# Kernel tuning notes

Hardware: AMD Instinct MI355X
Metric: run time of the kernel (lower is better)

## Reference

```python
import jax, jax.numpy as jnp
import numpy as np


def setup_inputs() -> dict:
    key = jax.random.key(0)
    ks = jax.random.split(key, 10)
    B, S, I, H, O, L = 64, 512, 256, 1024, 256, 3
    sI = 1.0 / np.sqrt(I)
    sH = 1.0 / np.sqrt(H)
    return {
        "x": jax.random.normal(ks[0], (B, S, I), jnp.float32),
        "h0": jax.random.normal(ks[1], (B, L, H), jnp.float32) * 0.1,
        "Wx0": jax.random.normal(ks[2], (I, 3 * H), jnp.float32) * sI,
        "Wh0": jax.random.normal(ks[3], (H, 3 * H), jnp.float32) * sH,
        "bh0": jax.random.normal(ks[4], (3 * H,), jnp.float32) * sH,
        "Wx": jax.random.normal(ks[5], (L - 1, H, 3 * H), jnp.float32) * sH,
        "Wh": jax.random.normal(ks[6], (L - 1, H, 3 * H), jnp.float32) * sH,
        "bh": jax.random.normal(ks[7], (L - 1, 3 * H), jnp.float32) * sH,
        "Wy": jax.random.normal(ks[8], (H, O), jnp.float32) * sH,
        "by": jax.random.normal(ks[9], (O,), jnp.float32) * sH,
    }


def _gru_forward(x, h0, Wx0, Wh0, bh0, Wx, Wh, bh, Wy, by):
    B, S, I = x.shape
    L = h0.shape[1]
    H = Wh0.shape[0]
    # per-layer params; gate order in the fused 3H dim: [z, r, g]
    params = [(Wx0, Wh0, bh0)] + [(Wx[l], Wh[l], bh[l]) for l in range(L - 1)]

    def step(states, x_t):
        states = list(states)
        cur = x_t  # (B, in_dim of layer)
        for l in range(L):
            Wx_l, Wh_l, b_l = params[l]
            h_prev = states[l]  # (B, H)
            gx = cur @ Wx_l  # (B, 3H), no bias (w_x* has bias=False)
            xz, xr, xg = gx[:, :H], gx[:, H:2 * H], gx[:, 2 * H:]
            # z and r gates use h_prev directly; g gate uses r*h_prev
            gh_zr = h_prev @ Wh_l[:, :2 * H] + b_l[:2 * H]
            z = jax.nn.sigmoid(xz + gh_zr[:, :H])
            r = jax.nn.sigmoid(xr + gh_zr[:, H:])
            g = jnp.tanh(xg + (r * h_prev) @ Wh_l[:, 2 * H:] + b_l[2 * H:])
            h_new = z * h_prev + (1.0 - z) * g
            states[l] = h_new
            cur = h_new  # dropout=0 -> identity
        y_t = cur @ Wy + by  # (B, O)
        return tuple(states), y_t

    init_states = tuple(h0[:, l, :] for l in range(L))
    final_states, ys = jax.lax.scan(step, init_states, jnp.swapaxes(x, 0, 1))
    layer_output = jnp.swapaxes(ys, 0, 1)  # (B, S, O)
    hidden_state = jnp.stack(final_states, axis=1)  # (B, L, H)
    return layer_output, hidden_state


def reference(x, h0, Wx0, Wh0, bh0, Wx, Wh, bh, Wy, by):
    return _gru_forward(x, h0, Wx0, Wh0, bh0, Wx, Wh, bh, Wy, by)
```

## Files before the change

kernel.cpp:

```cpp
#include <hip/hip_runtime.h>
#include <hip/hip_bf16.h>

#define SB 64
#define SS 512
#define SI 256
#define SH 1024
#define SO 256
#define NL 3

typedef __attribute__((ext_vector_type(8))) short bf16x8;
typedef __attribute__((ext_vector_type(4))) float f32x4;

__device__ __forceinline__ unsigned short f2bf(float f) {
  unsigned int u = __float_as_uint(f);
  u += 0x7fff + ((u >> 16) & 1);
  return (unsigned short)(u >> 16);
}


__global__ void k_transpose(const float* __restrict__ src, unsigned short* __restrict__ dst,
                            int K, int N) {
  __shared__ float tile[32][33];
  int n0 = blockIdx.x * 32, k0 = blockIdx.y * 32;
  int tx = threadIdx.x & 31, ty = threadIdx.x >> 5;
  for (int i = ty; i < 32; i += 8)
    tile[i][tx] = src[(size_t)(k0 + i) * N + (n0 + tx)];
  __syncthreads();
  for (int i = ty; i < 32; i += 8)
    dst[(size_t)(n0 + i) * K + (k0 + tx)] = f2bf(tile[tx][i]);
}

__global__ void k_init_h(const float* __restrict__ h0, float* __restrict__ h_f32,
                         unsigned short* __restrict__ h_bf) {
  int idx = blockIdx.x * blockDim.x + threadIdx.x;
  if (idx >= NL * SB * SH) return;
  int l = idx >> 16; int rem = idx & 65535; int b = rem >> 10; int c = rem & 1023;
  float v = h0[((size_t)b * NL + l) * SH + c];
  h_f32[idx] = v;
  h_bf[idx] = f2bf(v);
}

__global__ void k_final(const float* __restrict__ h_f32, float* __restrict__ out) {
  int idx = blockIdx.x * blockDim.x + threadIdx.x;
  if (idx >= NL * SB * SH) return;
  int l = idx >> 16; int rem = idx & 65535; int b = rem >> 10; int c = rem & 1023;
  out[(size_t)SB * SS * SO + ((size_t)b * NL + l) * SH + c] = h_f32[idx];
}

template<int K>
__device__ __forceinline__ void gemm_k(const unsigned short* __restrict__ Ap,
                                       const unsigned short* __restrict__ Bp,
                                       f32x4& acc0, f32x4& acc1) {
#pragma unroll 8
  for (int k0 = 0; k0 < K; k0 += 64) {
    bf16x8 a0 = *(const bf16x8*)(Ap + k0);
    bf16x8 b0 = *(const bf16x8*)(Bp + k0);
    bf16x8 a1 = *(const bf16x8*)(Ap + k0 + 32);
    bf16x8 b1 = *(const bf16x8*)(Bp + k0 + 32);
    acc0 = __builtin_amdgcn_mfma_f32_16x16x32_bf16(a0, b0, acc0, 0, 0, 0);
    acc1 = __builtin_amdgcn_mfma_f32_16x16x32_bf16(a1, b1, acc1, 0, 0, 0);
  }
}

__global__ __launch_bounds__(256) void k_stageA(
    int s,
    const float* __restrict__ x,
    const unsigned short* __restrict__ Wx0t,
    const unsigned short* __restrict__ Wx1t,
    const unsigned short* __restrict__ Wx2t,
    const unsigned short* __restrict__ Wh0t,
    const unsigned short* __restrict__ Wh1t,
    const unsigned short* __restrict__ Wh2t,
    const unsigned short* __restrict__ Wyt,
    const float* __restrict__ bh0,
    const float* __restrict__ bhx,
    const float* __restrict__ by,
    const unsigned short* __restrict__ h_bf,
    const float* __restrict__ h_f32,
    float* __restrict__ z_f32,
    unsigned short* __restrict__ rh_bf,
    float* __restrict__ gxg_f32,
    float* __restrict__ out) {
  const int tid  = threadIdx.x;
  const int wid  = tid >> 6;
  const int lane = tid & 63;
  const int lrow = lane & 15;
  const int kg   = lane >> 4;
  const int row0 = wid << 4;
  const int blk  = blockIdx.x;

  f32x4 acc0 = {0.f, 0.f, 0.f, 0.f};
  f32x4 acc1 = {0.f, 0.f, 0.f, 0.f};

  if (blk < 576) {
    const int l  = blk / 192;
    const int c0 = (blk % 192) << 4;
    const int t  = s - l;
    if (t < 0 || t >= SS) return;
    const int col = c0 + lrow;

    const unsigned short* Wht = (l == 0) ? Wh0t : ((l == 1) ? Wh1t : Wh2t);
    const float* bias = (l == 0) ? bh0 : (bhx + (size_t)(l - 1) * 3 * SH);

    if (l == 0) {
      const float* Ax = x + ((size_t)(row0 + lrow) * SS + t) * SI + kg * 8;
      const unsigned short* Bp = Wx0t + (size_t)col * SI + kg * 8;
#pragma unroll
      for (int k0 = 0; k0 < SI; k0 += 64) {
        bf16x8 a0, a1;
        const float* A0 = Ax + k0;
        const float* A1 = Ax + k0 + 32;
#pragma unroll
        for (int q = 0; q < 8; ++q) {
          a0[q] = (short)f2bf(A0[q]);
          a1[q] = (short)f2bf(A1[q]);
        }
        bf16x8 b0 = *(const bf16x8*)(Bp + k0);
        bf16x8 b1 = *(const bf16x8*)(Bp + k0 + 32);
        acc0 = __builtin_amdgcn_mfma_f32_16x16x32_bf16(a0, b0, acc0, 0, 0, 0);
        acc1 = __builtin_amdgcn_mfma_f32_16x16x32_bf16(a1, b1, acc1, 0, 0, 0);
      }
    } else {
      const unsigned short* curh = h_bf + (size_t)(l - 1) * SB * SH;
      const unsigned short* Wxt  = (l == 1) ? Wx1t : Wx2t;
      gemm_k<SH>(curh + (size_t)(row0 + lrow) * SH + kg * 8,
                 Wxt + (size_t)col * SH + kg * 8, acc0, acc1);
    }

    if (c0 < 2 * SH) {
      const unsigned short* hb = h_bf + (size_t)l * SB * SH;
      gemm_k<SH>(hb + (size_t)(row0 + lrow) * SH + kg * 8,
                 Wht + (size_t)col * SH + kg * 8, acc0, acc1);
      const float bsum = bias[col];
      const float* hf = h_f32 + (size_t)l * SB * SH;
#pragma unroll
      for (int j = 0; j < 4; ++j) {
        const int row = row0 + kg * 4 + j;
        const float v = acc0[j] + acc1[j] + bsum;
        const float sg = 1.f / (1.f + __expf(-v));
        if (col < SH) {
          z_f32[((size_t)l * SB + row) * SH + col] = sg;
        } else {
          const int cg = col - SH;
          const float hp = hf[(size_t)row * SH + cg];
          rh_bf[((size_t)l * SB + row) * SH + cg] = f2bf(sg * hp);
        }
      }
    } else {
      const int cg = col - 2 * SH;
#pragma unroll
      for (int j = 0; j < 4; ++j) {
        const int row = row0 + kg * 4 + j;
        gxg_f32[((size_t)l * SB + row) * SH + cg] = acc0[j] + acc1[j];
      }
    }
  } else {
    const int ty = s - 3;
    if (ty < 0 || ty >= SS) return;
    const int c0  = (blk - 576) << 4;
    const int col = c0 + lrow;
    const unsigned short* h2 = h_bf + (size_t)2 * SB * SH;
    gemm_k<SH>(h2 + (size_t)(row0 + lrow) * SH + kg * 8,
               Wyt + (size_t)col * SH + kg * 8, acc0, acc1);
    const float bsum = by[col];
#pragma unroll
    for (int j = 0; j < 4; ++j) {
      const int row = row0 + kg * 4 + j;
      out[((size_t)row * SS + ty) * SO + col] = acc0[j] + acc1[j] + bsum;
    }
  }
}

__global__ __launch_bounds__(256) void k_stageB(
    int s,
    const unsigned short* __restrict__ Wh0t,
    const unsigned short* __restrict__ Wh1t,
    const unsigned short* __restrict__ Wh2t,
    const float* __restrict__ bh0,
    const float* __restrict__ bhx,
    const unsigned short* __restrict__ rh_bf,
    const float* __restrict__ z_f32,
    const float* __restrict__ gxg_f32,
    float* __restrict__ h_f32,
    unsigned short* __restrict__ h_bf) {
  const int tid  = threadIdx.x;
  const int wid  = tid >> 6;
  const int lane = tid & 63;
  const int lrow = lane & 15;
  const int kg   = lane >> 4;
  const int row0 = wid << 4;
  const int blk  = blockIdx.x;
  const int l    = blk >> 6;
  const int c0   = (blk & 63) << 4;
  const int t    = s - l;
  if (t < 0 || t >= SS) return;

  const unsigned short* Wht = (l == 0) ? Wh0t : ((l == 1) ? Wh1t : Wh2t);
  const float* bias = (l == 0) ? bh0 : (bhx + (size_t)(l - 1) * 3 * SH);
  const int col = c0 + lrow;

  f32x4 acc0 = {0.f, 0.f, 0.f, 0.f};
  f32x4 acc1 = {0.f, 0.f, 0.f, 0.f};
  const unsigned short* rh = rh_bf + (size_t)l * SB * SH;
  gemm_k<SH>(rh + (size_t)(row0 + lrow) * SH + kg * 8,
             Wht + ((size_t)(2 * SH + col)) * SH + kg * 8, acc0, acc1);

  const float bsum = bias[2 * SH + col];
#pragma unroll
  for (int j = 0; j < 4; ++j) {
    const int row = row0 + kg * 4 + j;
    const size_t idx = ((size_t)l * SB + row) * SH + col;
    float v = acc0[j] + acc1[j] + gxg_f32[idx] + bsum;
    float e = __expf(2.f * v);
    float g = 1.f - 2.f / (e + 1.f);
    float z = z_f32[idx];
    float hp = h_f32[idx];
    float hn = z * hp + (1.f - z) * g;
    h_f32[idx] = hn;
    h_bf[idx] = f2bf(hn);
  }
}

extern "C" void kernel_launch(void* const* d_in, const int* in_sizes, int n_in,
                              void* d_out, int out_size, void* d_ws, size_t ws_size,
                              hipStream_t stream) {
  (void)in_sizes; (void)n_in; (void)out_size; (void)ws_size;
  const float* x   = (const float*)d_in[0];
  const float* h0  = (const float*)d_in[1];
  const float* Wx0 = (const float*)d_in[2];
  const float* Wh0 = (const float*)d_in[3];
  const float* bh0 = (const float*)d_in[4];
  const float* Wx  = (const float*)d_in[5];
  const float* Wh  = (const float*)d_in[6];
  const float* bh  = (const float*)d_in[7];
  const float* Wy  = (const float*)d_in[8];
  const float* by  = (const float*)d_in[9];
  float* out = (float*)d_out;

  char* p = (char*)d_ws;
  auto take = [&](size_t bytes) {
    char* r = p;
    p += (bytes + 255) & ~(size_t)255;
    return r;
  };
  unsigned short* Wx0t = (unsigned short*)take((size_t)3 * SH * SI * 2);
  unsigned short* Wx1t = (unsigned short*)take((size_t)3 * SH * SH * 2);
  unsigned short* Wx2t = (unsigned short*)take((size_t)3 * SH * SH * 2);
  unsigned short* Wh0t = (unsigned short*)take((size_t)3 * SH * SH * 2);
  unsigned short* Wh1t = (unsigned short*)take((size_t)3 * SH * SH * 2);
  unsigned short* Wh2t = (unsigned short*)take((size_t)3 * SH * SH * 2);
  unsigned short* Wyt  = (unsigned short*)take((size_t)SO * SH * 2);
  unsigned short* h_bf = (unsigned short*)take((size_t)NL * SB * SH * 2);
  unsigned short* rh_bf = (unsigned short*)take((size_t)NL * SB * SH * 2);
  float* h_f32   = (float*)take((size_t)NL * SB * SH * 4);
  float* z_f32   = (float*)take((size_t)NL * SB * SH * 4);
  float* gxg_f32 = (float*)take((size_t)NL * SB * SH * 4);

  k_transpose<<<dim3(3 * SH / 32, SI / 32), 256, 0, stream>>>(Wx0, Wx0t, SI, 3 * SH);
  k_transpose<<<dim3(3 * SH / 32, SH / 32), 256, 0, stream>>>(Wx, Wx1t, SH, 3 * SH);
  k_transpose<<<dim3(3 * SH / 32, SH / 32), 256, 0, stream>>>(Wx + (size_t)SH * 3 * SH, Wx2t, SH, 3 * SH);
  k_transpose<<<dim3(3 * SH / 32, SH / 32), 256, 0, stream>>>(Wh0, Wh0t, SH, 3 * SH);
  k_transpose<<<dim3(3 * SH / 32, SH / 32), 256, 0, stream>>>(Wh, Wh1t, SH, 3 * SH);
  k_transpose<<<dim3(3 * SH / 32, SH / 32), 256, 0, stream>>>(Wh + (size_t)SH * 3 * SH, Wh2t, SH, 3 * SH);
  k_transpose<<<dim3(SO / 32, SH / 32), 256, 0, stream>>>(Wy, Wyt, SH, SO);
  k_init_h<<<(NL * SB * SH) / 256, 256, 0, stream>>>(h0, h_f32, h_bf);

  for (int s = 0; s <= SS + 2; ++s) {
    k_stageA<<<592, 256, 0, stream>>>(s, x, Wx0t, Wx1t, Wx2t, Wh0t, Wh1t, Wh2t, Wyt,
                                      bh0, bh, by, h_bf, h_f32, z_f32, rh_bf, gxg_f32, out);
    if (s <= SS + 1)
      k_stageB<<<192, 256, 0, stream>>>(s, Wh0t, Wh1t, Wh2t, bh0, bh,
                                        rh_bf, z_f32, gxg_f32, h_f32, h_bf);
  }
  k_final<<<(NL * SB * SH) / 256, 256, 0, stream>>>(h_f32, out);
}
```

Measured before the change: 23.36 ms.

## Replace per-step kernel launches with one persistent kernel using grid barriers

Replaces the roughly one thousand alternating stage-A and stage-B launches with a single persistent kernel of 256 blocks. It statically assigns the 592 stage-A tiles and 192 stage-B tiles across those blocks and separates phases with an atomic-counter grid barrier. The final hidden-state copy is folded into the same kernel. The aim is to remove launch overhead and inter-kernel gaps on the latency-bound recurrence, at the cost of uneven per-block work, spin-wait barrier latency, and reliance on all 256 blocks being co-resident. It also lowers the GEMM inner-loop unroll factor.

Measured after the change: 38.25 ms. +63.8%, slower.

```diff
diff --git a/kernel.cpp b/kernel.cpp
--- a/kernel.cpp
+++ b/kernel.cpp
@@ -7,6 +7,9 @@
 #define SH 1024
 #define SO 256
 #define NL 3
+
+#define PBLK 256
+#define PTHR 256
 
 typedef __attribute__((ext_vector_type(8))) short bf16x8;
 typedef __attribute__((ext_vector_type(4))) float f32x4;
@@ -40,18 +43,11 @@
   h_bf[idx] = f2bf(v);
 }
 
-__global__ void k_final(const float* __restrict__ h_f32, float* __restrict__ out) {
-  int idx = blockIdx.x * blockDim.x + threadIdx.x;
-  if (idx >= NL * SB * SH) return;
-  int l = idx >> 16; int rem = idx & 65535; int b = rem >> 10; int c = rem & 1023;
-  out[(size_t)SB * SS * SO + ((size_t)b * NL + l) * SH + c] = h_f32[idx];
-}
-
 template<int K>
 __device__ __forceinline__ void gemm_k(const unsigned short* __restrict__ Ap,
                                        const unsigned short* __restrict__ Bp,
                                        f32x4& acc0, f32x4& acc1) {
-#pragma unroll 8
+#pragma unroll 4
   for (int k0 = 0; k0 < K; k0 += 64) {
     bf16x8 a0 = *(const bf16x8*)(Ap + k0);
     bf16x8 b0 = *(const bf16x8*)(Bp + k0);
@@ -62,49 +58,62 @@
   }
 }
 
-__global__ __launch_bounds__(256) void k_stageA(
-    int s,
-    const float* __restrict__ x,
-    const unsigned short* __restrict__ Wx0t,
-    const unsigned short* __restrict__ Wx1t,
-    const unsigned short* __restrict__ Wx2t,
-    const unsigned short* __restrict__ Wh0t,
-    const unsigned short* __restrict__ Wh1t,
-    const unsigned short* __restrict__ Wh2t,
-    const unsigned short* __restrict__ Wyt,
-    const float* __restrict__ bh0,
-    const float* __restrict__ bhx,
-    const float* __restrict__ by,
-    const unsigned short* __restrict__ h_bf,
-    const float* __restrict__ h_f32,
-    float* __restrict__ z_f32,
-    unsigned short* __restrict__ rh_bf,
-    float* __restrict__ gxg_f32,
-    float* __restrict__ out) {
-  const int tid  = threadIdx.x;
-  const int wid  = tid >> 6;
-  const int lane = tid & 63;
-  const int lrow = lane & 15;
-  const int kg   = lane >> 4;
-  const int row0 = wid << 4;
-  const int blk  = blockIdx.x;
-
+
+struct GruArgs {
+  const float* x;
+  const unsigned short* Wx0t;
+  const unsigned short* Wx1t;
+  const unsigned short* Wx2t;
+  const unsigned short* Wh0t;
+  const unsigned short* Wh1t;
+  const unsigned short* Wh2t;
+  const unsigned short* Wyt;
+  const float* bh0;
+  const float* bhx;
+  const float* by;
+  unsigned short* h_bf;
+  unsigned short* rh_bf;
+  float* h_f32;
+  float* z_f32;
+  float* gxg_f32;
+  float* out;
+  unsigned* bar;
+};
+
+__device__ __forceinline__ void gbar(unsigned* arrive, unsigned* release, unsigned epoch) {
+  __syncthreads();
+  if (threadIdx.x == 0) {
+    __threadfence();
+    unsigned prev = __hip_atomic_fetch_add(arrive, 1u, __ATOMIC_ACQ_REL,
+                                           __HIP_MEMORY_SCOPE_AGENT);
+    if (prev == epoch * PBLK + (PBLK - 1))
+      __hip_atomic_store(release, epoch + 1u, __ATOMIC_RELEASE,
+                         __HIP_MEMORY_SCOPE_AGENT);
+    while (__hip_atomic_load(release, __ATOMIC_RELAXED,
+                             __HIP_MEMORY_SCOPE_AGENT) < epoch + 1u)
+      __builtin_amdgcn_s_sleep(2);
+    __threadfence();
+  }
+  __syncthreads();
+}
+
+__device__ __forceinline__ void do_tileA(const GruArgs& A, int ta, int s,
+                                         int row0, int lrow, int kg) {
   f32x4 acc0 = {0.f, 0.f, 0.f, 0.f};
   f32x4 acc1 = {0.f, 0.f, 0.f, 0.f};
-
-  if (blk < 576) {
-    const int l  = blk / 192;
-    const int c0 = (blk % 192) << 4;
+  if (ta < 576) {
+    const int l  = ta / 192;
+    const int c0 = (ta % 192) << 4;
     const int t  = s - l;
     if (t < 0 || t >= SS) return;
     const int col = c0 + lrow;
-
-    const unsigned short* Wht = (l == 0) ? Wh0t : ((l == 1) ? Wh1t : Wh2t);
-    const float* bias = (l == 0) ? bh0 : (bhx + (size_t)(l - 1) * 3 * SH);
+    const unsigned short* Wxt = (l == 0) ? A.Wx0t : ((l == 1) ? A.Wx1t : A.Wx2t);
+    const unsigned short* Wht = (l == 0) ? A.Wh0t : ((l == 1) ? A.Wh1t : A.Wh2t);
+    const float* bias = (l == 0) ? A.bh0 : (A.bhx + (size_t)(l - 1) * 3 * SH);
 
     if (l == 0) {
-      const float* Ax = x + ((size_t)(row0 + lrow) * SS + t) * SI + kg * 8;
-      const unsigned short* Bp = Wx0t + (size_t)col * SI + kg * 8;
+      const float* Ax = A.x + ((size_t)(row0 + lrow) * SS + t) * SI + kg * 8;
+      const unsigned short* Bp = Wxt + (size_t)col * SI + kg * 8;
 #pragma unroll
       for (int k0 = 0; k0 < SI; k0 += 64) {
         bf16x8 a0, a1;
@@ -121,29 +130,28 @@
         acc1 = __builtin_amdgcn_mfma_f32_16x16x32_bf16(a1, b1, acc1, 0, 0, 0);
       }
     } else {
-      const unsigned short* curh = h_bf + (size_t)(l - 1) * SB * SH;
-      const unsigned short* Wxt  = (l == 1) ? Wx1t : Wx2t;
+      const unsigned short* curh = A.h_bf + (size_t)(l - 1) * SB * SH;
       gemm_k<SH>(curh + (size_t)(row0 + lrow) * SH + kg * 8,
                  Wxt + (size_t)col * SH + kg * 8, acc0, acc1);
     }
 
     if (c0 < 2 * SH) {
-      const unsigned short* hb = h_bf + (size_t)l * SB * SH;
+      const unsigned short* hb = A.h_bf + (size_t)l * SB * SH;
       gemm_k<SH>(hb + (size_t)(row0 + lrow) * SH + kg * 8,
                  Wht + (size_t)col * SH + kg * 8, acc0, acc1);
       const float bsum = bias[col];
-      const float* hf = h_f32 + (size_t)l * SB * SH;
+      const float* hf = A.h_f32 + (size_t)l * SB * SH;
 #pragma unroll
       for (int j = 0; j < 4; ++j) {
         const int row = row0 + kg * 4 + j;
         const float v = acc0[j] + acc1[j] + bsum;
         const float sg = 1.f / (1.f + __expf(-v));
         if (col < SH) {
-          z_f32[((size_t)l * SB + row) * SH + col] = sg;
+          A.z_f32[((size_t)l * SB + row) * SH + col] = sg;
         } else {
           const int cg = col - SH;
           const float hp = hf[(size_t)row * SH + cg];
-          rh_bf[((size_t)l * SB + row) * SH + cg] = f2bf(sg * hp);
+          A.rh_bf[((size_t)l * SB + row) * SH + cg] = f2bf(sg * hp);
         }
       }
     } else {
@@ -151,38 +159,59 @@
 #pragma unroll
       for (int j = 0; j < 4; ++j) {
         const int row = row0 + kg * 4 + j;
-        gxg_f32[((size_t)l * SB + row) * SH + cg] = acc0[j] + acc1[j];
+        A.gxg_f32[((size_t)l * SB + row) * SH + cg] = acc0[j] + acc1[j];
       }
     }
   } else {
     const int ty = s - 3;
     if (ty < 0 || ty >= SS) return;
-    const int c0  = (blk - 576) << 4;
+    const int c0  = (ta - 576) << 4;
     const int col = c0 + lrow;
-    const unsigned short* h2 = h_bf + (size_t)2 * SB * SH;
+    const unsigned short* h2 = A.h_bf + (size_t)2 * SB * SH;
     gemm_k<SH>(h2 + (size_t)(row0 + lrow) * SH + kg * 8,
-               Wyt + (size_t)col * SH + kg * 8, acc0, acc1);
-    const float bsum = by[col];
+               A.Wyt + (size_t)col * SH + kg * 8, acc0, acc1);
+    const float bsum = A.by[col];
 #pragma unroll
     for (int j = 0; j < 4; ++j) {
       const int row = row0 + kg * 4 + j;
-      out[((size_t)row * SS + ty) * SO + col] = acc0[j] + acc1[j] + bsum;
+      A.out[((size_t)row * SS + ty) * SO + col] = acc0[j] + acc1[j] + bsum;
     }
   }
 }
 
-__global__ __launch_bounds__(256) void k_stageB(
-    int s,
-    const unsigned short* __restrict__ Wh0t,
-    const unsigned short* __restrict__ Wh1t,
-    const unsigned short* __restrict__ Wh2t,
-    const float* __restrict__ bh0,
-    const float* __restrict__ bhx,
-    const unsigned short* __restrict__ rh_bf,
-    const float* __restrict__ z_f32,
-    const float* __restrict__ gxg_f32,
-    float* __restrict__ h_f32,
-    unsigned short* __restrict__ h_bf) {
+__device__ __forceinline__ void do_tileB(const GruArgs& A, int tb, int s,
+                                         int row0, int lrow, int kg) {
+  const int lb  = tb >> 6;
+  const int cb0 = (tb & 63) << 4;
+  const int t   = s - lb;
+  if (t < 0 || t >= SS) return;
+  const unsigned short* Wht = (lb == 0) ? A.Wh0t : ((lb == 1) ? A.Wh1t : A.Wh2t);
+  const float* bias = (lb == 0) ? A.bh0 : (A.bhx + (size_t)(lb - 1) * 3 * SH);
+  const int col = cb0 + lrow;
+
+  f32x4 acc0 = {0.f, 0.f, 0.f, 0.f};
+  f32x4 acc1 = {0.f, 0.f, 0.f, 0.f};
+  const unsigned short* rh = A.rh_bf + (size_t)lb * SB * SH;
+  gemm_k<SH>(rh + (size_t)(row0 + lrow) * SH + kg * 8,
+             Wht + ((size_t)(2 * SH + col)) * SH + kg * 8, acc0, acc1);
+
+  const float bsum = bias[2 * SH + col];
+#pragma unroll
+  for (int j = 0; j < 4; ++j) {
+    const int row = row0 + kg * 4 + j;
+    const size_t idx = ((size_t)lb * SB + row) * SH + col;
+    float v = acc0[j] + acc1[j] + A.gxg_f32[idx] + bsum;
+    float e = __expf(2.f * v);
+    float g = 1.f - 2.f / (e + 1.f);
+    float z = A.z_f32[idx];
+    float hp = A.h_f32[idx];
+    float hn = z * hp + (1.f - z) * g;
+    A.h_f32[idx] = hn;
+    A.h_bf[idx] = f2bf(hn);
+  }
+}
+
+__global__ __launch_bounds__(PTHR, 2) void k_gru(GruArgs A) {
   const int tid  = threadIdx.x;
   const int wid  = tid >> 6;
   const int lane = tid & 63;
@@ -190,34 +219,28 @@
   const int kg   = lane >> 4;
   const int row0 = wid << 4;
   const int blk  = blockIdx.x;
-  const int l    = blk >> 6;
-  const int c0   = (blk & 63) << 4;
-  const int t    = s - l;
-  if (t < 0 || t >= SS) return;
-
-  const unsigned short* Wht = (l == 0) ? Wh0t : ((l == 1) ? Wh1t : Wh2t);
-  const float* bias = (l == 0) ? bh0 : (bhx + (size_t)(l - 1) * 3 * SH);
-  const int col = c0 + lrow;
-
-  f32x4 acc0 = {0.f, 0.f, 0.f, 0.f};
-  f32x4 acc1 = {0.f, 0.f, 0.f, 0.f};
-  const unsigned short* rh = rh_bf + (size_t)l * SB * SH;
-  gemm_k<SH>(rh + (size_t)(row0 + lrow) * SH + kg * 8,
-             Wht + ((size_t)(2 * SH + col)) * SH + kg * 8, acc0, acc1);
-
-  const float bsum = bias[2 * SH + col];
-#pragma unroll
-  for (int j = 0; j < 4; ++j) {
-    const int row = row0 + kg * 4 + j;
-    const size_t idx = ((size_t)l * SB + row) * SH + col;
-    float v = acc0[j] + acc1[j] + gxg_f32[idx] + bsum;
-    float e = __expf(2.f * v);
-    float g = 1.f - 2.f / (e + 1.f);
-    float z = z_f32[idx];
-    float hp = h_f32[idx];
-    float hn = z * hp + (1.f - z) * g;
-    h_f32[idx] = hn;
-    h_bf[idx] = f2bf(hn);
+  unsigned* arrive  = A.bar;
+  unsigned* release = A.bar + 32;
+
+  int t0, t1, t2 = -1;
+  if (blk < 64)        { t0 = 192 + blk; t1 = 128 + blk; t2 = 320 + blk; }
+  else if (blk < 80)   { int i = blk - 64; t0 = 256 + i; t1 = 512 + 2 * i; t2 = 513 + 2 * i; }
+  else if (blk < 128)  { int j = blk - 80; t0 = 272 + j; t1 = (j < 32) ? 544 + j : 576 + (j - 32); }
+  else                 { int m = blk - 128; t0 = 384 + m; t1 = m; }
+
+  unsigned epoch = 0;
+  for (int s = 0; s <= SS + 2; ++s) {
+    do_tileA(A, t0, s, row0, lrow, kg);
+    do_tileA(A, t1, s, row0, lrow, kg);
+    if (t2 >= 0) do_tileA(A, t2, s, row0, lrow, kg);
+    gbar(arrive, release, epoch++);
+    if (blk < 192) do_tileB(A, blk, s, row0, lrow, kg);
+    gbar(arrive, release, epoch++);
+  }
+
+  for (int idx = blk * PTHR + tid; idx < NL * SB * SH; idx += PBLK * PTHR) {
+    int l2 = idx >> 16; int rem = idx & 65535; int b = rem >> 10; int c = rem & 1023;
+    A.out[(size_t)SB * SS * SO + ((size_t)b * NL + l2) * SH + c] = A.h_f32[idx];
   }
 }
 
@@ -255,6 +278,9 @@
   float* h_f32   = (float*)take((size_t)NL * SB * SH * 4);
   float* z_f32   = (float*)take((size_t)NL * SB * SH * 4);
   float* gxg_f32 = (float*)take((size_t)NL * SB * SH * 4);
+  unsigned* bar  = (unsigned*)take(256);
+
+  hipMemsetAsync(bar, 0, 256, stream);
 
   k_transpose<<<dim3(3 * SH / 32, SI / 32), 256, 0, stream>>>(Wx0, Wx0t, SI, 3 * SH);
   k_transpose<<<dim3(3 * SH / 32, SH / 32), 256, 0, stream>>>(Wx, Wx1t, SH, 3 * SH);
@@ -265,12 +291,16 @@
   k_transpose<<<dim3(SO / 32, SH / 32), 256, 0, stream>>>(Wy, Wyt, SH, SO);
   k_init_h<<<(NL * SB * SH) / 256, 256, 0, stream>>>(h0, h_f32, h_bf);
 
-  for (int s = 0; s <= SS + 2; ++s) {
-    k_stageA<<<592, 256, 0, stream>>>(s, x, Wx0t, Wx1t, Wx2t, Wh0t, Wh1t, Wh2t, Wyt,
-                                      bh0, bh, by, h_bf, h_f32, z_f32, rh_bf, gxg_f32, out);
-    if (s <= SS + 1)
-      k_stageB<<<192, 256, 0, stream>>>(s, Wh0t, Wh1t, Wh2t, bh0, bh,
-                                        rh_bf, z_f32, gxg_f32, h_f32, h_bf);
-  }
-  k_final<<<(NL * SB * SH) / 256, 256, 0, stream>>>(h_f32, out);
-}
+  GruArgs args;
+  args.x = x;
+  args.Wx0t = Wx0t; args.Wx1t = Wx1t; args.Wx2t = Wx2t;
+  args.Wh0t = Wh0t; args.Wh1t = Wh1t; args.Wh2t = Wh2t;
+  args.Wyt = Wyt;
+  args.bh0 = bh0; args.bhx = bh; args.by = by;
+  args.h_bf = h_bf; args.rh_bf = rh_bf;
+  args.h_f32 = h_f32; args.z_f32 = z_f32; args.gxg_f32 = gxg_f32;
+  args.out = out;
+  args.bar = bar;
+
+  k_gru<<<PBLK, PTHR, 0, stream>>>(args);
+}
```
